# Optimization experiments

Hardware: AMD Instinct MI355X
Metric: run time of the kernel (lower is better)

## Reference

```python
import jax, jax.numpy as jnp
import numpy as np

B, S, D, H = 2, 2048, 2048, 16
HD = D // H


def setup_inputs() -> dict:
    key = jax.random.key(0)
    ks = jax.random.split(key, 11)
    scale = 1.0 / np.sqrt(D)
    causal = jnp.tril(jnp.ones((S, S), dtype=bool))
    attention_mask = jnp.broadcast_to(causal, (B, H, S, S))
    return {
        "queries": jax.random.normal(ks[0], (B, S, D), dtype=jnp.float32),
        "keys": jax.random.normal(ks[1], (B, S, D), dtype=jnp.float32),
        "values": jax.random.normal(ks[2], (B, S, D), dtype=jnp.float32),
        "attention_mask": attention_mask,
        "wq": jax.random.normal(ks[3], (D, D), dtype=jnp.float32) * scale,
        "bq": jax.random.normal(ks[4], (D,), dtype=jnp.float32) * 0.01,
        "wk": jax.random.normal(ks[5], (D, D), dtype=jnp.float32) * scale,
        "bk": jax.random.normal(ks[6], (D,), dtype=jnp.float32) * 0.01,
        "wv": jax.random.normal(ks[7], (D, D), dtype=jnp.float32) * scale,
        "bv": jax.random.normal(ks[8], (D,), dtype=jnp.float32) * 0.01,
        "wo": jax.random.normal(ks[9], (D, D), dtype=jnp.float32) * scale,
        "bo": jax.random.normal(ks[10], (D,), dtype=jnp.float32) * 0.01,
    }


def _split_heads(x):
    # (B, S, D) -> (B, H, S, HD)
    b, s, _ = x.shape
    return x.reshape(b, s, H, HD).transpose(0, 2, 1, 3)


def reference(queries, keys, values, attention_mask, wq, bq, wk, bk, wv, bv, wo, bo):
    # Linear layers (torch convention: x @ W.T + b)
    q = _split_heads(queries @ wq.T + bq)   # (B, H, S, HD)
    k = _split_heads(keys @ wk.T + bk)
    v = _split_heads(values @ wv.T + bv)

    inv_sqrt_d = 1.0 / jnp.sqrt(jnp.asarray(HD, dtype=q.dtype))
    scores = jnp.einsum('bhqd,bhkd->bhqk', q, k) * inv_sqrt_d  # (B, H, S, S)
    scores = jnp.where(attention_mask, scores, jnp.asarray(-jnp.inf, dtype=scores.dtype))
    probs = jax.nn.softmax(scores, axis=-1)
    out = jnp.einsum('bhqk,bhkd->bhqd', probs, v)              # (B, H, S, HD)

    out = out.transpose(0, 2, 1, 3).reshape(queries.shape[0], queries.shape[1], D)
    return out @ wo.T + bo
```

## Files before the change

### kernel.cpp

```cpp
#include <hip/hip_runtime.h>
#include <hip/hip_bf16.h>

typedef unsigned short u16;
typedef __bf16 bf16x8 __attribute__((ext_vector_type(8)));
typedef short  short8 __attribute__((ext_vector_type(8)));
typedef float  f32x4  __attribute__((ext_vector_type(4)));
typedef float  f32x16 __attribute__((ext_vector_type(16)));
typedef u16    u16x4  __attribute__((ext_vector_type(4)));
typedef unsigned uintx2 __attribute__((ext_vector_type(2)));

#define BB 2
#define SS 2048
#define DD 2048
#define HH 16
#define HDIM 128
#define MM (BB * SS)
#define KSCALE 0.12752039505554602f

static __device__ __forceinline__ f32x4 mfma16(short8 a, short8 b, f32x4 c) {
    return __builtin_amdgcn_mfma_f32_16x16x32_bf16(
        __builtin_bit_cast(bf16x8, a), __builtin_bit_cast(bf16x8, b), c, 0, 0, 0);
}

static __device__ __forceinline__ f32x16 mfma32(short8 a, short8 b, f32x16 c) {
    return __builtin_amdgcn_mfma_f32_32x32x16_bf16(
        __builtin_bit_cast(bf16x8, a), __builtin_bit_cast(bf16x8, b), c, 0, 0, 0);
}

static __device__ __forceinline__ u16 f2bf(float f) {
    union { float f; unsigned u; } v; v.f = f;
    unsigned r = v.u + 0x7fffu + ((v.u >> 16) & 1u);
    return (u16)(r >> 16);
}

static __device__ __forceinline__ float bf2f(u16 v) {
    union { unsigned u; float f; } t; t.u = ((unsigned)v) << 16;
    return t.f;
}

static __device__ __forceinline__ unsigned cvtpk(float lo, float hi) {
    unsigned r;
    asm("v_cvt_pk_bf16_f32 %0, %1, %2" : "=v"(r) : "v"(lo), "v"(hi));
    return r;
}

static __device__ __forceinline__ void plswap(unsigned &a, unsigned &b) {
    asm("v_permlane32_swap_b32 %0, %1" : "+v"(a), "+v"(b));
}

static __device__ __forceinline__ uint4 pack8(float4 a, float4 b) {
    uint4 o;
    o.x = (unsigned)f2bf(a.x) | ((unsigned)f2bf(a.y) << 16);
    o.y = (unsigned)f2bf(a.z) | ((unsigned)f2bf(a.w) << 16);
    o.z = (unsigned)f2bf(b.x) | ((unsigned)f2bf(b.y) << 16);
    o.w = (unsigned)f2bf(b.z) | ((unsigned)f2bf(b.w) << 16);
    return o;
}

static __device__ __forceinline__ void gload_lds16(const u16* g, u16* l) {
    __builtin_amdgcn_global_load_lds(
        (const __attribute__((address_space(1))) unsigned int*)g,
        (__attribute__((address_space(3))) unsigned int*)l, 16, 0, 0);
}

__global__ __launch_bounds__(256) void conv_all(
    const float* __restrict__ q, const float* __restrict__ k, const float* __restrict__ v,
    const float* __restrict__ wq, const float* __restrict__ wk,
    const float* __restrict__ wv, const float* __restrict__ wo,
    u16* __restrict__ out)
{
    constexpr int n1 = MM * DD / 8;
    constexpr int nw = DD * DD / 8;
    constexpr int total = 3 * n1 + 4 * nw;
    const int stride = gridDim.x * blockDim.x;
    for (int i = blockIdx.x * blockDim.x + threadIdx.x; i < total; i += stride) {
        const float* s; int j = i; float sc = 1.f;
        if (j < n1)            { s = q; }
        else if (j < 2 * n1)   { s = k;  j -= n1; }
        else if (j < 3 * n1)   { s = v;  j -= 2 * n1; }
        else {
            j -= 3 * n1;
            if (j < nw)        { s = wq; sc = KSCALE; }
            else if (j < 2*nw) { s = wk; j -= nw; }
            else if (j < 3*nw) { s = wv; j -= 2 * nw; }
            else               { s = wo; j -= 3 * nw; }
        }
        const float4* sp = (const float4*)s + (size_t)j * 2;
        float4 a = sp[0], bb2 = sp[1];
        a.x *= sc; a.y *= sc; a.z *= sc; a.w *= sc;
        bb2.x *= sc; bb2.y *= sc; bb2.z *= sc; bb2.w *= sc;
        ((uint4*)out)[i] = pack8(a, bb2);
    }
}

__global__ __launch_bounds__(256, 3) void gemm_qkv(
    const u16* __restrict__ A0, const u16* __restrict__ W0,
    const float* __restrict__ bq, const float* __restrict__ bk,
    const float* __restrict__ bv, u16* __restrict__ C0)
{
    __shared__ u16 S[128 * 132];
    u16* Al = S;
    u16* Bl = S + 4096;

    const int z = blockIdx.z;
    const u16* A  = A0 + (size_t)z * MM * DD;
    const u16* Wb = W0 + (size_t)z * DD * DD;
    const float* bias = (z == 0) ? bq : (z == 1 ? bk : bv);
    const float bsc = (z == 0) ? KSCALE : 1.f;

    const int tid = threadIdx.x;
    const int lane = tid & 63;
    const int lg = lane >> 4, li = lane & 15;
    const int wid = tid >> 6;
    const int brow = blockIdx.x * 128, bcol = blockIdx.y * 128;
    const int wm = wid >> 1, wn = wid & 1;

    const int srow = tid >> 2;
    const int scol = (tid & 3) * 8;

    const f32x4 zero = {0.f, 0.f, 0.f, 0.f};
    f32x4 acc[4][4];
#pragma unroll
    for (int i = 0; i < 4; ++i)
#pragma unroll
        for (int j = 0; j < 4; ++j) acc[i][j] = zero;

    const u16* aptr = A  + (size_t)(brow + srow) * DD + scol;
    const u16* bptr = Wb + (size_t)(bcol + srow) * DD + scol;
    const size_t half = (size_t)64 * DD;

    for (int kt = 0; kt < DD; kt += 32) {
        gload_lds16(aptr + kt,        &Al[tid * 8]);
        gload_lds16(aptr + half + kt, &Al[2048 + tid * 8]);
        gload_lds16(bptr + kt,        &Bl[tid * 8]);
        gload_lds16(bptr + half + kt, &Bl[2048 + tid * 8]);
        __syncthreads();

        short8 af[4], bf[4];
#pragma unroll
        for (int mi = 0; mi < 4; ++mi)
            af[mi] = *(const short8*)(&Al[(wm * 64 + mi * 16 + li) * 32 + lg * 8]);
#pragma unroll
        for (int ni = 0; ni < 4; ++ni)
            bf[ni] = *(const short8*)(&Bl[(wn * 64 + ni * 16 + li) * 32 + lg * 8]);
#pragma unroll
        for (int mi = 0; mi < 4; ++mi)
#pragma unroll
            for (int ni = 0; ni < 4; ++ni)
                acc[mi][ni] = mfma16(af[mi], bf[ni], acc[mi][ni]);
        __syncthreads();
    }

    if (z == 2) {
        u16* Cl = S;
#pragma unroll
        for (int ni = 0; ni < 4; ++ni) {
            const int cc = wn * 64 + ni * 16 + li;
            const float bvv = bias[bcol + cc];
#pragma unroll
            for (int mi = 0; mi < 4; ++mi)
#pragma unroll
                for (int r = 0; r < 4; ++r) {
                    const int rr = wm * 64 + mi * 16 + lg * 4 + r;
                    Cl[cc * 132 + rr] = f2bf(acc[mi][ni][r] + bvv);
                }
        }
        __syncthreads();
        const int row = tid >> 1;
        const int hcol = (tid & 1) * 64;
        u16* dst = C0 + (size_t)2 * MM * DD + (size_t)(bcol + row) * MM + brow + hcol;
#pragma unroll
        for (int c = 0; c < 8; ++c)
            *(short8*)(dst + c * 8) = *(const short8*)(&Cl[row * 132 + hcol + c * 8]);
    } else {
        u16* Cp = C0 + (size_t)z * MM * DD;
#pragma unroll
        for (int ni = 0; ni < 4; ++ni) {
            const int col = bcol + wn * 64 + ni * 16 + li;
            const float bvv = bias[col] * bsc;
#pragma unroll
            for (int mi = 0; mi < 4; ++mi)
#pragma unroll
                for (int r = 0; r < 4; ++r) {
                    const int row = brow + wm * 64 + mi * 16 + lg * 4 + r;
                    Cp[(size_t)row * DD + col] = f2bf(acc[mi][ni][r] + bvv);
                }
        }
    }
}

__global__ __launch_bounds__(256) void gemm_out(
    const u16* __restrict__ A, const u16* __restrict__ Wb,
    const float* __restrict__ bias, float* __restrict__ Cp)
{
    __shared__ u16 Al[128 * 32];
    __shared__ u16 Bl[128 * 32];

    const int tid = threadIdx.x;
    const int lane = tid & 63;
    const int lg = lane >> 4, li = lane & 15;
    const int wid = tid >> 6;
    const int brow = blockIdx.x * 128, bcol = blockIdx.y * 128;
    const int wm = wid >> 1, wn = wid & 1;

    const int srow = tid >> 2;
    const int scol = (tid & 3) * 8;

    const f32x4 zero = {0.f, 0.f, 0.f, 0.f};
    f32x4 acc[4][4];
#pragma unroll
    for (int i = 0; i < 4; ++i)
#pragma unroll
        for (int j = 0; j < 4; ++j) acc[i][j] = zero;

    const u16* aptr = A  + (size_t)(brow + srow) * DD + scol;
    const u16* bptr = Wb + (size_t)(bcol + srow) * DD + scol;
    const size_t half = (size_t)64 * DD;

    for (int kt = 0; kt < DD; kt += 32) {
        gload_lds16(aptr + kt,        &Al[tid * 8]);
        gload_lds16(aptr + half + kt, &Al[2048 + tid * 8]);
        gload_lds16(bptr + kt,        &Bl[tid * 8]);
        gload_lds16(bptr + half + kt, &Bl[2048 + tid * 8]);
        __syncthreads();

        short8 af[4], bf[4];
#pragma unroll
        for (int mi = 0; mi < 4; ++mi)
            af[mi] = *(const short8*)(&Al[(wm * 64 + mi * 16 + li) * 32 + lg * 8]);
#pragma unroll
        for (int ni = 0; ni < 4; ++ni)
            bf[ni] = *(const short8*)(&Bl[(wn * 64 + ni * 16 + li) * 32 + lg * 8]);
#pragma unroll
        for (int mi = 0; mi < 4; ++mi)
#pragma unroll
            for (int ni = 0; ni < 4; ++ni)
                acc[mi][ni] = mfma16(af[mi], bf[ni], acc[mi][ni]);
        __syncthreads();
    }

#pragma unroll
    for (int ni = 0; ni < 4; ++ni) {
        const int col = bcol + wn * 64 + ni * 16 + li;
        const float bvv = bias[col];
#pragma unroll
        for (int mi = 0; mi < 4; ++mi)
#pragma unroll
            for (int r = 0; r < 4; ++r) {
                const int row = brow + wm * 64 + mi * 16 + lg * 4 + r;
                Cp[(size_t)row * DD + col] = acc[mi][ni][r] + bvv;
            }
    }
}

__global__ __launch_bounds__(256) void flash_attn(
    const u16* __restrict__ Q, const u16* __restrict__ Kp,
    const u16* __restrict__ Vt, u16* __restrict__ O,
    u16* __restrict__ PartO, float* __restrict__ PartML)
{
    __shared__ u16 lds[16384];
    u16* Kl = lds;
    u16* Vl = lds + 8192;

    const int tid = threadIdx.x;
    const int wid = tid >> 6, lane = tid & 63;
    const int l5 = lane & 31;
    const int hi = lane >> 5;
    const int h = blockIdx.y, b = blockIdx.z;

    const int f = 39 - (int)blockIdx.x;
    int qt, ch;
    if (f < 4)       { qt = f;               ch = 0; }
    else if (f < 12) { int g = f - 4;  qt = 4  + (g >> 1); ch = g & 1; }
    else if (f < 24) { int g = f - 12; qt = 8  + g / 3;    ch = g % 3; }
    else             { int g = f - 24; qt = 12 + (g >> 2); ch = g & 3; }
    const int j0 = ch * 8;
    const int j1 = min(j0 + 8, 2 * qt + 2);
    const int qbase = qt * 128 + wid * 32;
    const int qg = qbase + l5;

    const int rK0 = tid >> 4, wK0 = tid & 15;
    const int bK0 = ((wK0 * 16) ^ ((rK0 & 7) << 4)) >> 1;
    const int rV0 = tid >> 3, wV0 = tid & 7;
    const int bV0 = ((wV0 * 16) ^ ((rV0 & 7) << 4)) >> 1;
    const u16* kbase = Kp + (size_t)(b * SS + rK0) * DD + h * HDIM + bK0;
    const u16* vbase = Vt + (size_t)(h * HDIM + rV0) * MM + b * SS + bV0;

    short8 qf[8];
    {
        const u16* qp0 = Q + (size_t)(b * SS + qg) * DD + h * HDIM + hi * 8;
#pragma unroll
        for (int ks = 0; ks < 8; ++ks)
            qf[ks] = *(const short8*)(qp0 + ks * 16);
    }

    float m_r = -__builtin_inff(), l_r = 0.f;
    f32x16 accO[4];
#pragma unroll
    for (int d = 0; d < 4; ++d) accO[d] = (f32x16)(0.f);

    for (int j = j0; j < j1; ++j) {
#pragma unroll
        for (int i_ = 0; i_ < 4; ++i_) {
            gload_lds16(kbase + (size_t)(j * 64 + i_ * 16) * DD, &Kl[(i_ * 256 + tid) * 8]);
            gload_lds16(vbase + (size_t)(i_ * 32) * MM + j * 64, &Vl[(i_ * 256 + tid) * 8]);
        }
        __syncthreads();

        if (j * 64 <= qbase + 31) {
            f32x16 accS[2];
            accS[0] = (f32x16)(0.f); accS[1] = (f32x16)(0.f);
            __builtin_amdgcn_s_setprio(1);
#pragma unroll
            for (int ks = 0; ks < 8; ++ks) {
#pragma unroll
                for (int kvb = 0; kvb < 2; ++kvb) {
                    const int row = kvb * 32 + l5;
                    const int e = (ks * 16 + hi * 8) ^ ((row & 7) << 3);
                    short8 kf = *(const short8*)(&Kl[row * 128 + e]);
                    accS[kvb] = mfma32(kf, qf[ks], accS[kvb]);
                }
            }
            __builtin_amdgcn_s_setprio(0);

            const bool domask = (j * 64 + 63 > qbase);
            float rmax = -__builtin_inff();
            if (domask) {
#pragma unroll
                for (int kvb = 0; kvb < 2; ++kvb)
#pragma unroll
                    for (int r = 0; r < 16; ++r) {
                        float t = accS[kvb][r];
                        const int kv = j * 64 + kvb * 32 + (r & 3) + 8 * (r >> 2) + 4 * hi;
                        if (kv > qg) t = -__builtin_inff();
                        accS[kvb][r] = t;
                        rmax = fmaxf(rmax, t);
                    }
            } else {
#pragma unroll
                for (int kvb = 0; kvb < 2; ++kvb)
#pragma unroll
                    for (int r = 0; r < 16; ++r)
                        rmax = fmaxf(rmax, accS[kvb][r]);
            }
            rmax = fmaxf(rmax, __shfl_xor(rmax, 32, 64));

            if (!__all(rmax - m_r <= 11.5f)) {
                const float mn = fmaxf(m_r, rmax);
                const float sf = exp2f(m_r - mn);
                m_r = mn;
                l_r *= sf;
#pragma unroll
                for (int db = 0; db < 4; ++db) accO[db] = accO[db] * sf;
            }

            float ls = 0.f;
#pragma unroll
            for (int kvb = 0; kvb < 2; ++kvb)
#pragma unroll
                for (int r = 0; r < 16; ++r) {
                    const float e = exp2f(accS[kvb][r] - m_r);
                    accS[kvb][r] = e;
                    ls += e;
                }
            ls += __shfl_xor(ls, 32, 64);
            l_r += ls;

            __builtin_amdgcn_s_setprio(1);
#pragma unroll
            for (int ks = 0; ks < 4; ++ks) {
                const int kvb = ks >> 1;
                const int r0 = (ks & 1) * 8;
                unsigned x0 = cvtpk(accS[kvb][r0 + 0], accS[kvb][r0 + 1]);
                unsigned y0 = cvtpk(accS[kvb][r0 + 2], accS[kvb][r0 + 3]);
                unsigned x1 = cvtpk(accS[kvb][r0 + 4], accS[kvb][r0 + 5]);
                unsigned y1 = cvtpk(accS[kvb][r0 + 6], accS[kvb][r0 + 7]);
                plswap(x0, x1);
                plswap(y0, y1);
                union { unsigned u[4]; short8 s; } pf;
                pf.u[0] = x0; pf.u[1] = y0; pf.u[2] = x1; pf.u[3] = y1;
#pragma unroll
                for (int db = 0; db < 4; ++db) {
                    const int row = db * 32 + l5;
                    const int e = (ks * 16 + hi * 8) ^ ((row & 7) << 3);
                    short8 vf = *(const short8*)(&Vl[row * 64 + e]);
                    accO[db] = mfma32(vf, pf.s, accO[db]);
                }
            }
            __builtin_amdgcn_s_setprio(0);
        }
        __syncthreads();
    }

    if (f >= 4) {
        const int pslot = (b * HH + h) * 36 + (f - 4);
        u16* po = PartO + (size_t)pslot * 16384 + (size_t)(wid * 32 + l5) * 128;
#pragma unroll
        for (int db = 0; db < 4; ++db)
#pragma unroll
            for (int g = 0; g < 4; ++g) {
                const int d0 = db * 32 + g * 8 + hi * 4;
                uintx2 pk;
                pk.x = cvtpk(accO[db][g * 4 + 0], accO[db][g * 4 + 1]);
                pk.y = cvtpk(accO[db][g * 4 + 2], accO[db][g * 4 + 3]);
                *(uintx2*)(po + d0) = pk;
            }
        if (lane < 32) {
            float* ml = PartML + (size_t)pslot * 256;
            ml[wid * 32 + l5]       = m_r;
            ml[128 + wid * 32 + l5] = l_r;
        }
    } else {
        const float linv = 1.f / l_r;
        u16* Wl = lds + wid * 4096;
#pragma unroll
        for (int db = 0; db < 4; ++db)
#pragma unroll
            for (int g = 0; g < 4; ++g) {
                const int d0 = db * 32 + g * 8 + hi * 4;
                uintx2 pk;
                pk.x = cvtpk(accO[db][g * 4 + 0] * linv, accO[db][g * 4 + 1] * linv);
                pk.y = cvtpk(accO[db][g * 4 + 2] * linv, accO[db][g * 4 + 3] * linv);
                *(uintx2*)(&Wl[l5 * 128 + (d0 ^ ((l5 & 7) << 4))]) = pk;
            }
        const int q_l = lane >> 1;
        const int d0r = (lane & 1) * 64;
        u16* op = O + (size_t)(b * SS + qt * 128 + wid * 32 + q_l) * DD + h * HDIM + d0r;
#pragma unroll
        for (int c = 0; c < 8; ++c) {
            short8 vv = *(const short8*)(&Wl[q_l * 128 + ((d0r + c * 8) ^ ((q_l & 7) << 4))]);
            *(short8*)(op + c * 8) = vv;
        }
    }
}

__global__ __launch_bounds__(256) void attn_combine(
    const u16* __restrict__ PartO, const float* __restrict__ PartML,
    u16* __restrict__ O)
{
    const int qt = 4 + (int)blockIdx.x;
    const int h = blockIdx.y, b = blockIdx.z;
    const int nch = qt / 4 + 1;
    int f0m4;
    if (qt < 8)       f0m4 = (qt - 4) * 2;
    else if (qt < 12) f0m4 = 8 + (qt - 8) * 3;
    else              f0m4 = 20 + (qt - 12) * 4;
    const int pbase = (b * HH + h) * 36 + f0m4;

    const int tid = threadIdx.x;
    const int q = tid & 127;
    const int d0 = (tid >> 7) * 64;

    float mc[4], lc[4];
#pragma unroll
    for (int c = 0; c < 4; ++c) {
        if (c < nch) {
            mc[c] = PartML[(size_t)(pbase + c) * 256 + q];
            lc[c] = PartML[(size_t)(pbase + c) * 256 + 128 + q];
        } else { mc[c] = -__builtin_inff(); lc[c] = 0.f; }
    }
    float M = fmaxf(fmaxf(mc[0], mc[1]), fmaxf(mc[2], mc[3]));
    float wc[4], L = 0.f;
#pragma unroll
    for (int c = 0; c < 4; ++c) { wc[c] = exp2f(mc[c] - M); L += wc[c] * lc[c]; }
    const float Linv = 1.f / L;

    float acc[64];
#pragma unroll
    for (int i = 0; i < 64; ++i) acc[i] = 0.f;
#pragma unroll
    for (int c = 0; c < 4; ++c) {
        if (c < nch) {
            const float w = wc[c] * Linv;
            const u16* po = PartO + (size_t)(pbase + c) * 16384 + (size_t)q * 128 + d0;
#pragma unroll
            for (int i = 0; i < 64; ++i)
                acc[i] += w * bf2f(po[i]);
        }
    }

    u16* op = O + (size_t)(b * SS + qt * 128 + q) * DD + h * HDIM + d0;
#pragma unroll
    for (int j = 0; j < 8; ++j) {
        short8 vv;
#pragma unroll
        for (int e = 0; e < 8; ++e) vv[e] = (short)f2bf(acc[j * 8 + e]);
        *(short8*)(op + j * 8) = vv;
    }
}

extern "C" void kernel_launch(void* const* d_in, const int* in_sizes, int n_in,
                              void* d_out, int out_size, void* d_ws, size_t ws_size,
                              hipStream_t stream)
{
    const float* queries = (const float*)d_in[0];
    const float* keys    = (const float*)d_in[1];
    const float* values  = (const float*)d_in[2];
    const float* wq = (const float*)d_in[4];
    const float* bq = (const float*)d_in[5];
    const float* wk = (const float*)d_in[6];
    const float* bk = (const float*)d_in[7];
    const float* wv = (const float*)d_in[8];
    const float* bv = (const float*)d_in[9];
    const float* wo = (const float*)d_in[10];
    const float* bo = (const float*)d_in[11];

    const int NMD = MM * DD;
    const int NWW = DD * DD;

    u16* qb  = (u16*)d_ws;
    u16* wqb = qb  + (size_t)3 * NMD;
    u16* wob = wqb + (size_t)3 * NWW;
    u16* qw  = wob + (size_t)NWW;
    u16* aw  = qw  + (size_t)3 * NMD;
    u16*   partO  = qb;
    float* partML = (float*)wqb;
    (void)in_sizes; (void)n_in; (void)out_size; (void)ws_size;

    dim3 blk(256);
    dim3 gridC(2048);
    dim3 gridQKV(MM / 128, DD / 128, 3);
    dim3 gridO(MM / 128, DD / 128);
    dim3 gridA(40, HH, BB);
    dim3 gridX(12, HH, BB);

    conv_all<<<gridC, blk, 0, stream>>>(queries, keys, values, wq, wk, wv, wo, qb);
    gemm_qkv<<<gridQKV, blk, 0, stream>>>(qb, wqb, bq, bk, bv, qw);
    flash_attn<<<gridA, blk, 0, stream>>>(qw, qw + (size_t)NMD, qw + (size_t)2 * NMD, aw,
                                          partO, partML);
    attn_combine<<<gridX, blk, 0, stream>>>(partO, partML, aw);
    gemm_out<<<gridO, blk, 0, stream>>>(aw, wob, bo, (float*)d_out);
}
```

Before: 329.4 us.

## Rewrite QKV GEMM with triple-buffered async LDS pipeline, 8 waves, swizzled tiles

The QKV projection GEMM moves from a single-buffered 256-thread loop with two barriers per 32-wide k-step to a 512-thread block with a three-stage LDS ring buffer over 64-wide k-steps. Global-to-LDS loads run two stages ahead, synchronised with vmcnt waits and one barrier per step. LDS columns are XOR-swizzled to avoid bank conflicts, and s_setprio is raised around the MFMA block. The aim is to hide global load latency and cut barrier overhead, at the cost of more LDS per block (96 KB), which limits occupancy.

```diff
diff --git a/kernel.cpp b/kernel.cpp
--- a/kernel.cpp
+++ b/kernel.cpp
@@ -93,20 +93,144 @@
     }
 }
 
-__global__ __launch_bounds__(256, 3) void gemm_qkv(
+__global__ __launch_bounds__(512) void gemm_qkv(
     const u16* __restrict__ A0, const u16* __restrict__ W0,
     const float* __restrict__ bq, const float* __restrict__ bk,
     const float* __restrict__ bv, u16* __restrict__ C0)
 {
-    __shared__ u16 S[128 * 132];
-    u16* Al = S;
-    u16* Bl = S + 4096;
+    __shared__ u16 Ab[3][8192];
+    __shared__ u16 Bb[3][8192];
 
     const int z = blockIdx.z;
     const u16* A  = A0 + (size_t)z * MM * DD;
     const u16* Wb = W0 + (size_t)z * DD * DD;
     const float* bias = (z == 0) ? bq : (z == 1 ? bk : bv);
     const float bsc = (z == 0) ? KSCALE : 1.f;
+
+    const int tid = threadIdx.x;
+    const int lane = tid & 63;
+    const int lg = lane >> 4, li = lane & 15;
+    const int wid = tid >> 6;
+    const int wr = wid >> 2, wc = wid & 3;
+    const int brow = blockIdx.x * 128, bcol = blockIdx.y * 128;
+    const int K = DD;
+
+    const int srow = tid >> 3;
+    const int schunk = ((tid & 7) * 8) ^ ((srow & 7) << 3);
+    const u16* aS = A  + (size_t)(brow + srow) * K + schunk;
+    const u16* bS = Wb + (size_t)(bcol + srow) * K + schunk;
+
+#define STAGE_Q(T, BUF) do {                                                   \
+        gload_lds16(aS + (size_t)(T) * 64,                &Ab[BUF][tid * 8]);  \
+        gload_lds16(aS + (size_t)64 * K + (size_t)(T)*64, &Ab[BUF][4096 + tid * 8]); \
+        gload_lds16(bS + (size_t)(T) * 64,                &Bb[BUF][tid * 8]);  \
+        gload_lds16(bS + (size_t)64 * K + (size_t)(T)*64, &Bb[BUF][4096 + tid * 8]); \
+    } while (0)
+
+    const f32x4 zero = {0.f, 0.f, 0.f, 0.f};
+    f32x4 acc[4][2];
+#pragma unroll
+    for (int i = 0; i < 4; ++i) { acc[i][0] = zero; acc[i][1] = zero; }
+
+    const int swz = (li & 7) << 3;
+    const int c0 = (lg * 8) ^ swz;
+    const int c1 = (32 + lg * 8) ^ swz;
+    int aoff[4], boff[2];
+#pragma unroll
+    for (int mi = 0; mi < 4; ++mi) aoff[mi] = (wr * 64 + mi * 16 + li) * 64;
+#pragma unroll
+    for (int ni = 0; ni < 2; ++ni) boff[ni] = (wc * 32 + ni * 16 + li) * 64;
+
+    STAGE_Q(0, 0);
+    STAGE_Q(1, 1);
+    asm volatile("s_waitcnt vmcnt(4)" ::: "memory");
+    __builtin_amdgcn_s_barrier();
+    __builtin_amdgcn_sched_barrier(0);
+
+    int bufc = 0;
+    for (int t = 0; t < 32; ++t) {
+        if (t < 30) {
+            const int bn = (t + 2) - ((t + 2) / 3) * 3;
+            STAGE_Q(t + 2, bn);
+        }
+
+        const u16* Ac = Ab[bufc];
+        const u16* Bc = Bb[bufc];
+        short8 af[4][2], bf[2][2];
+#pragma unroll
+        for (int mi = 0; mi < 4; ++mi) {
+            af[mi][0] = *(const short8*)(&Ac[aoff[mi] + c0]);
+            af[mi][1] = *(const short8*)(&Ac[aoff[mi] + c1]);
+        }
+#pragma unroll
+        for (int ni = 0; ni < 2; ++ni) {
+            bf[ni][0] = *(const short8*)(&Bc[boff[ni] + c0]);
+            bf[ni][1] = *(const short8*)(&Bc[boff[ni] + c1]);
+        }
+        __builtin_amdgcn_s_setprio(1);
+#pragma unroll
+        for (int mi = 0; mi < 4; ++mi)
+#pragma unroll
+            for (int ni = 0; ni < 2; ++ni) {
+                acc[mi][ni] = mfma16(af[mi][0], bf[ni][0], acc[mi][ni]);
+                acc[mi][ni] = mfma16(af[mi][1], bf[ni][1], acc[mi][ni]);
+            }
+        __builtin_amdgcn_s_setprio(0);
+
+        if (t < 30)       asm volatile("s_waitcnt vmcnt(4)" ::: "memory");
+        else if (t == 30) asm volatile("s_waitcnt vmcnt(0)" ::: "memory");
+        if (t < 31) {
+            __builtin_amdgcn_s_barrier();
+            __builtin_amdgcn_sched_barrier(0);
+        }
+        bufc = (bufc == 2) ? 0 : bufc + 1;
+    }
+#undef STAGE_Q
+
+    if (z == 2) {
+        __syncthreads();
+        u16* Wl = &Ab[0][0] + wid * 2176;
+#pragma unroll
+        for (int ni = 0; ni < 2; ++ni) {
+            const int cc = ni * 16 + li;
+            const float bvv = bias[bcol + wc * 32 + cc];
+#pragma unroll
+            for (int mi = 0; mi < 4; ++mi)
+#pragma unroll
+                for (int r = 0; r < 4; ++r)
+                    Wl[cc * 68 + mi * 16 + lg * 4 + r] = f2bf(acc[mi][ni][r] + bvv);
+        }
+        __builtin_amdgcn_s_barrier();
+        const int d = lane >> 1;
+        const int mh = (lane & 1) * 32;
+        u16* dst = C0 + (size_t)2 * MM * DD +
+                   (size_t)(bcol + wc * 32 + d) * MM + brow + wr * 64 + mh;
+#pragma unroll
+        for (int c = 0; c < 4; ++c)
+            *(short8*)(dst + c * 8) = *(const short8*)(&Wl[d * 68 + mh + c * 8]);
+    } else {
+        u16* Cp = C0 + (size_t)z * MM * DD;
+#pragma unroll
+        for (int ni = 0; ni < 2; ++ni) {
+            const int col = bcol + wc * 32 + ni * 16 + li;
+            const float bvv = bias[col] * bsc;
+#pragma unroll
+            for (int mi = 0; mi < 4; ++mi)
+#pragma unroll
+                for (int r = 0; r < 4; ++r) {
+                    const int row = brow + wr * 64 + mi * 16 + lg * 4 + r;
+                    Cp[(size_t)row * DD + col] = f2bf(acc[mi][ni][r] + bvv);
+                }
+        }
+    }
+}
+
+__global__ __launch_bounds__(256) void gemm_out(
+    const u16* __restrict__ A, const u16* __restrict__ Wb,
+    const float* __restrict__ bias, float* __restrict__ Cp)
+{
+    __shared__ u16 Al[128 * 32];
+    __shared__ u16 Bl[128 * 32];
 
     const int tid = threadIdx.x;
     const int lane = tid & 63;
@@ -115,104 +239,15 @@
     const int brow = blockIdx.x * 128, bcol = blockIdx.y * 128;
     const int wm = wid >> 1, wn = wid & 1;
 
+    const f32x4 zero = {0.f, 0.f, 0.f, 0.f};
+    f32x4 acc[4][4];
+#pragma unroll
+    for (int i = 0; i < 4; ++i)
+#pragma unroll
+        for (int j = 0; j < 4; ++j) acc[i][j] = zero;
+
     const int srow = tid >> 2;
     const int scol = (tid & 3) * 8;
-
-    const f32x4 zero = {0.f, 0.f, 0.f, 0.f};
-    f32x4 acc[4][4];
-#pragma unroll
-    for (int i = 0; i < 4; ++i)
-#pragma unroll
-        for (int j = 0; j < 4; ++j) acc[i][j] = zero;
-
-    const u16* aptr = A  + (size_t)(brow + srow) * DD + scol;
-    const u16* bptr = Wb + (size_t)(bcol + srow) * DD + scol;
-    const size_t half = (size_t)64 * DD;
-
-    for (int kt = 0; kt < DD; kt += 32) {
-        gload_lds16(aptr + kt,        &Al[tid * 8]);
-        gload_lds16(aptr + half + kt, &Al[2048 + tid * 8]);
-        gload_lds16(bptr + kt,        &Bl[tid * 8]);
-        gload_lds16(bptr + half + kt, &Bl[2048 + tid * 8]);
-        __syncthreads();
-
-        short8 af[4], bf[4];
-#pragma unroll
-        for (int mi = 0; mi < 4; ++mi)
-            af[mi] = *(const short8*)(&Al[(wm * 64 + mi * 16 + li) * 32 + lg * 8]);
-#pragma unroll
-        for (int ni = 0; ni < 4; ++ni)
-            bf[ni] = *(const short8*)(&Bl[(wn * 64 + ni * 16 + li) * 32 + lg * 8]);
-#pragma unroll
-        for (int mi = 0; mi < 4; ++mi)
-#pragma unroll
-            for (int ni = 0; ni < 4; ++ni)
-                acc[mi][ni] = mfma16(af[mi], bf[ni], acc[mi][ni]);
-        __syncthreads();
-    }
-
-    if (z == 2) {
-        u16* Cl = S;
-#pragma unroll
-        for (int ni = 0; ni < 4; ++ni) {
-            const int cc = wn * 64 + ni * 16 + li;
-            const float bvv = bias[bcol + cc];
-#pragma unroll
-            for (int mi = 0; mi < 4; ++mi)
-#pragma unroll
-                for (int r = 0; r < 4; ++r) {
-                    const int rr = wm * 64 + mi * 16 + lg * 4 + r;
-                    Cl[cc * 132 + rr] = f2bf(acc[mi][ni][r] + bvv);
-                }
-        }
-        __syncthreads();
-        const int row = tid >> 1;
-        const int hcol = (tid & 1) * 64;
-        u16* dst = C0 + (size_t)2 * MM * DD + (size_t)(bcol + row) * MM + brow + hcol;
-#pragma unroll
-        for (int c = 0; c < 8; ++c)
-            *(short8*)(dst + c * 8) = *(const short8*)(&Cl[row * 132 + hcol + c * 8]);
-    } else {
-        u16* Cp = C0 + (size_t)z * MM * DD;
-#pragma unroll
-        for (int ni = 0; ni < 4; ++ni) {
-            const int col = bcol + wn * 64 + ni * 16 + li;
-            const float bvv = bias[col] * bsc;
-#pragma unroll
-            for (int mi = 0; mi < 4; ++mi)
-#pragma unroll
-                for (int r = 0; r < 4; ++r) {
-                    const int row = brow + wm * 64 + mi * 16 + lg * 4 + r;
-                    Cp[(size_t)row * DD + col] = f2bf(acc[mi][ni][r] + bvv);
-                }
-        }
-    }
-}
-
-__global__ __launch_bounds__(256) void gemm_out(
-    const u16* __restrict__ A, const u16* __restrict__ Wb,
-    const float* __restrict__ bias, float* __restrict__ Cp)
-{
-    __shared__ u16 Al[128 * 32];
-    __shared__ u16 Bl[128 * 32];
-
-    const int tid = threadIdx.x;
-    const int lane = tid & 63;
-    const int lg = lane >> 4, li = lane & 15;
-    const int wid = tid >> 6;
-    const int brow = blockIdx.x * 128, bcol = blockIdx.y * 128;
-    const int wm = wid >> 1, wn = wid & 1;
-
-    const int srow = tid >> 2;
-    const int scol = (tid & 3) * 8;
-
-    const f32x4 zero = {0.f, 0.f, 0.f, 0.f};
-    f32x4 acc[4][4];
-#pragma unroll
-    for (int i = 0; i < 4; ++i)
-#pragma unroll
-        for (int j = 0; j < 4; ++j) acc[i][j] = zero;
-
     const u16* aptr = A  + (size_t)(brow + srow) * DD + scol;
     const u16* bptr = Wb + (size_t)(bcol + srow) * DD + scol;
     const size_t half = (size_t)64 * DD;
@@ -518,6 +553,7 @@
     (void)in_sizes; (void)n_in; (void)out_size; (void)ws_size;
 
     dim3 blk(256);
+    dim3 blkG(512);
     dim3 gridC(2048);
     dim3 gridQKV(MM / 128, DD / 128, 3);
     dim3 gridO(MM / 128, DD / 128);
@@ -525,7 +561,7 @@
     dim3 gridX(12, HH, BB);
 
     conv_all<<<gridC, blk, 0, stream>>>(queries, keys, values, wq, wk, wv, wo, qb);
-    gemm_qkv<<<gridQKV, blk, 0, stream>>>(qb, wqb, bq, bk, bv, qw);
+    gemm_qkv<<<gridQKV, blkG, 0, stream>>>(qb, wqb, bq, bk, bv, qw);
     flash_attn<<<gridA, blk, 0, stream>>>(qw, qw + (size_t)NMD, qw + (size_t)2 * NMD, aw,
                                           partO, partML);
     attn_combine<<<gridX, blk, 0, stream>>>(partO, partML, aw);
```

New measurement: 399.4 us. +21.3%, slower.

## Rebalance flash-attention split-KV chunks and map head groups to XCDs

Applied to the files above, without the earlier changes.

Changes the causal attention work split. Each query tile now gets roughly (2qt+7)/6 KV chunks of about three KV blocks each, giving 51 blocks per head instead of 40 and a more even per-block workload. Block indices are remapped so that the blocks of one batch/head group land on the same XCD, which should improve L2 reuse of K/V. In exchange, more partial outputs must be written and merged, and the combine kernel now handles up to 6 chunks across 13 query tiles.

```diff
diff --git a/kernel.cpp b/kernel.cpp
--- a/kernel.cpp
+++ b/kernel.cpp
@@ -203,16 +203,15 @@
     const int brow = blockIdx.x * 128, bcol = blockIdx.y * 128;
     const int wm = wid >> 1, wn = wid & 1;
 
+    const f32x4 zero = {0.f, 0.f, 0.f, 0.f};
+    f32x4 acc[4][4];
+#pragma unroll
+    for (int i = 0; i < 4; ++i)
+#pragma unroll
+        for (int j = 0; j < 4; ++j) acc[i][j] = zero;
+
     const int srow = tid >> 2;
     const int scol = (tid & 3) * 8;
-
-    const f32x4 zero = {0.f, 0.f, 0.f, 0.f};
-    f32x4 acc[4][4];
-#pragma unroll
-    for (int i = 0; i < 4; ++i)
-#pragma unroll
-        for (int j = 0; j < 4; ++j) acc[i][j] = zero;
-
     const u16* aptr = A  + (size_t)(brow + srow) * DD + scol;
     const u16* bptr = Wb + (size_t)(bcol + srow) * DD + scol;
     const size_t half = (size_t)64 * DD;
@@ -266,16 +265,20 @@
     const int wid = tid >> 6, lane = tid & 63;
     const int l5 = lane & 31;
     const int hi = lane >> 5;
-    const int h = blockIdx.y, b = blockIdx.z;
-
-    const int f = 39 - (int)blockIdx.x;
-    int qt, ch;
-    if (f < 4)       { qt = f;               ch = 0; }
-    else if (f < 12) { int g = f - 4;  qt = 4  + (g >> 1); ch = g & 1; }
-    else if (f < 24) { int g = f - 12; qt = 8  + g / 3;    ch = g % 3; }
-    else             { int g = f - 24; qt = 12 + (g >> 2); ch = g & 3; }
-    const int j0 = ch * 8;
-    const int j1 = min(j0 + 8, 2 * qt + 2);
+
+    const int lin = (int)blockIdx.x + 51 * ((int)blockIdx.y + 16 * (int)blockIdx.z);
+    const int xcd = lin & 7;
+    const int idx = lin >> 3;
+    const int grp = xcd + 8 * (idx & 3);
+    const int f   = idx >> 2;
+    const int b = grp >> 4, h = grp & 15;
+
+    int qt = 15, rem = f, C;
+    for (;;) { C = (2 * qt + 7) / 6; if (rem < C) break; rem -= C; --qt; }
+    const int ch = rem;
+    const int T = 2 * qt + 2;
+    const int j0 = ch * T / C;
+    const int j1 = (ch + 1) * T / C;
     const int qbase = qt * 128 + wid * 32;
     const int qg = qbase + l5;
 
@@ -392,8 +395,10 @@
         __syncthreads();
     }
 
-    if (f >= 4) {
-        const int pslot = (b * HH + h) * 36 + (f - 4);
+    if (C > 1) {
+        int sbase = 0;
+        for (int q2 = 3; q2 < qt; ++q2) sbase += (2 * q2 + 7) / 6;
+        const int pslot = grp * 48 + sbase + ch;
         u16* po = PartO + (size_t)pslot * 16384 + (size_t)(wid * 32 + l5) * 128;
 #pragma unroll
         for (int db = 0; db < 4; ++db)
@@ -438,38 +443,38 @@
     const u16* __restrict__ PartO, const float* __restrict__ PartML,
     u16* __restrict__ O)
 {
-    const int qt = 4 + (int)blockIdx.x;
+    const int qt = 3 + (int)blockIdx.x;
     const int h = blockIdx.y, b = blockIdx.z;
-    const int nch = qt / 4 + 1;
-    int f0m4;
-    if (qt < 8)       f0m4 = (qt - 4) * 2;
-    else if (qt < 12) f0m4 = 8 + (qt - 8) * 3;
-    else              f0m4 = 20 + (qt - 12) * 4;
-    const int pbase = (b * HH + h) * 36 + f0m4;
+    const int nch = (2 * qt + 7) / 6;
+    int sbase = 0;
+    for (int q2 = 3; q2 < qt; ++q2) sbase += (2 * q2 + 7) / 6;
+    const int pbase = (b * HH + h) * 48 + sbase;
 
     const int tid = threadIdx.x;
     const int q = tid & 127;
     const int d0 = (tid >> 7) * 64;
 
-    float mc[4], lc[4];
-#pragma unroll
-    for (int c = 0; c < 4; ++c) {
+    float mc[6], lc[6];
+#pragma unroll
+    for (int c = 0; c < 6; ++c) {
         if (c < nch) {
             mc[c] = PartML[(size_t)(pbase + c) * 256 + q];
             lc[c] = PartML[(size_t)(pbase + c) * 256 + 128 + q];
         } else { mc[c] = -__builtin_inff(); lc[c] = 0.f; }
     }
-    float M = fmaxf(fmaxf(mc[0], mc[1]), fmaxf(mc[2], mc[3]));
-    float wc[4], L = 0.f;
-#pragma unroll
-    for (int c = 0; c < 4; ++c) { wc[c] = exp2f(mc[c] - M); L += wc[c] * lc[c]; }
+    float M = mc[0];
+#pragma unroll
+    for (int c = 1; c < 6; ++c) M = fmaxf(M, mc[c]);
+    float wc[6], L = 0.f;
+#pragma unroll
+    for (int c = 0; c < 6; ++c) { wc[c] = exp2f(mc[c] - M); L += wc[c] * lc[c]; }
     const float Linv = 1.f / L;
 
     float acc[64];
 #pragma unroll
     for (int i = 0; i < 64; ++i) acc[i] = 0.f;
 #pragma unroll
-    for (int c = 0; c < 4; ++c) {
+    for (int c = 0; c < 6; ++c) {
         if (c < nch) {
             const float w = wc[c] * Linv;
             const u16* po = PartO + (size_t)(pbase + c) * 16384 + (size_t)q * 128 + d0;
@@ -521,8 +526,8 @@
     dim3 gridC(2048);
     dim3 gridQKV(MM / 128, DD / 128, 3);
     dim3 gridO(MM / 128, DD / 128);
-    dim3 gridA(40, HH, BB);
-    dim3 gridX(12, HH, BB);
+    dim3 gridA(51, HH, BB);
+    dim3 gridX(13, HH, BB);
 
     conv_all<<<gridC, blk, 0, stream>>>(queries, keys, values, wq, wk, wv, wo, qb);
     gemm_qkv<<<gridQKV, blk, 0, stream>>>(qb, wqb, bq, bk, bv, qw);
```

Result: no change. 333.2 us (+1.1%).
